# Performance work log

Hardware: AMD Instinct MI355X
Metric: run time of the kernel (lower is better)

The kernel has to match this reference:

```python
import jax, jax.numpy as jnp
import numpy as np

DIM = 2048
NUM_EXPERTS = 64
NUM_TOKENS = 16384
BETA = 0.5
EPSILON = 0.05
SINKHORN_ITER = 5
EPS_NORM = 1e-12  # torch F.normalize clamp


def setup_inputs() -> dict:
    key = jax.random.key(0)
    kx, ke = jax.random.split(key)
    x = jax.random.normal(kx, (NUM_TOKENS, DIM), dtype=jnp.float32)
    # orthogonal init for experts [E, dim]
    g = jax.random.normal(ke, (NUM_EXPERTS, DIM), dtype=jnp.float32)
    q, r = jnp.linalg.qr(g.T)  # [dim, E]
    experts = (q * jnp.sign(jnp.diag(r))).T  # [E, dim], orthonormal rows
    return {"x": x, "experts": experts}


def _l2_normalize(v, axis=-1):
    n = jnp.linalg.norm(v, axis=axis, keepdims=True)
    return v / jnp.maximum(n, EPS_NORM)


def _log_sinkhorn(cost, epsilon, iterations):
    B, E = cost.shape
    log_K = -cost / epsilon  # [B, E]
    log_col_mass = jnp.log(jnp.float32(B) / jnp.float32(E))

    def body(carry, _):
        log_u, log_v = carry
        log_u = -jax.nn.logsumexp(log_K + log_v[None, :], axis=1)  # [B]
        log_v = log_col_mass - jax.nn.logsumexp(log_K + log_u[:, None], axis=0)  # [E]
        return (log_u, log_v), None

    init = (jnp.zeros((B,), cost.dtype), jnp.zeros((E,), cost.dtype))
    (log_u, log_v), _ = jax.lax.scan(body, init, None, length=iterations)
    return log_K + log_u[:, None] + log_v[None, :]


def reference(x, experts):
    x_norm = _l2_normalize(x)          # [B, dim]
    e_norm = _l2_normalize(experts)    # [E, dim]
    sim = x_norm @ e_norm.T            # [B, E]
    gram = e_norm @ e_norm.T           # [E, E]
    gram_off = jax.nn.relu(gram - jnp.eye(NUM_EXPERTS, dtype=gram.dtype))
    repulsion = sim @ gram_off         # [B, E]
    score = sim - BETA * repulsion
    cost = -score
    log_P = _log_sinkhorn(cost, EPSILON, SINKHORN_ITER)
    probs = jnp.exp(log_P)
    return (probs, sim, gram, gram_off)
```

## Files before the change

kernel.cpp:

```cpp
#include <hip/hip_runtime.h>
#include <math.h>

#define TOKENS 16384
#define EXPERTS 64
#define DIM 2048
#define BETA 0.5f
#define EPSILON 0.05f
#define EPSN 1e-12f
#define LOGMASS 5.545177444479562f

#define OFF_ENORM   0
#define OFF_BBF     131072
#define OFF_M       262144
#define OFF_LOGK    266240
#define OFF_U       1314816
#define OFF_V       1331200
#define OFF_PART    1331264


typedef __attribute__((ext_vector_type(8))) short short8v;
typedef __attribute__((ext_vector_type(4))) float f32x4;

static __device__ __forceinline__ unsigned short f2bf(float f) {
  unsigned int u = __float_as_uint(f);
  u += 0x7FFFu + ((u >> 16) & 1u);
  return (unsigned short)(u >> 16);
}

__global__ __launch_bounds__(256) void k1_norm_experts(const float* __restrict__ ex,
                                                       float* __restrict__ ws) {
  int j = blockIdx.x, t = threadIdx.x;
  const float4* row4 = (const float4*)(ex + (size_t)j * DIM);
  float4 v0 = row4[t];
  float4 v1 = row4[t + 256];
  float ss = v0.x*v0.x + v0.y*v0.y + v0.z*v0.z + v0.w*v0.w
           + v1.x*v1.x + v1.y*v1.y + v1.z*v1.z + v1.w*v1.w;
  #pragma unroll
  for (int m = 1; m < 64; m <<= 1) ss += __shfl_xor(ss, m);
  __shared__ float red[4];
  int wv = t >> 6, ln = t & 63;
  if (ln == 0) red[wv] = ss;
  __syncthreads();
  float tot = red[0] + red[1] + red[2] + red[3];
  float sc = 1.0f / fmaxf(sqrtf(tot), EPSN);
  float4 w0 = make_float4(v0.x*sc, v0.y*sc, v0.z*sc, v0.w*sc);
  float4 w1 = make_float4(v1.x*sc, v1.y*sc, v1.z*sc, v1.w*sc);
  float4* en4 = (float4*)(ws + OFF_ENORM + (size_t)j * DIM);
  en4[t] = w0;
  en4[t + 256] = w1;
  unsigned short* Bb = (unsigned short*)(ws + OFF_BBF);
  int k0 = t * 4;
  int i0 = ((k0 >> 5) << 11) + (j << 5) + (k0 & 31);
  ushort4 u0; u0.x = f2bf(w0.x); u0.y = f2bf(w0.y); u0.z = f2bf(w0.z); u0.w = f2bf(w0.w);
  *(ushort4*)(Bb + i0) = u0;
  int k1v = (t + 256) * 4;
  int i1 = ((k1v >> 5) << 11) + (j << 5) + (k1v & 31);
  ushort4 u1; u1.x = f2bf(w1.x); u1.y = f2bf(w1.y); u1.z = f2bf(w1.z); u1.w = f2bf(w1.w);
  *(ushort4*)(Bb + i1) = u1;
}

__global__ __launch_bounds__(256) void k2_gram(const float* __restrict__ wsr,
                                               float* __restrict__ ws,
                                               float* __restrict__ out) {
  __shared__ __align__(16) float ej[DIM];
  __shared__ float part[4][64];
  int j = blockIdx.x, t = threadIdx.x;
  const float4* en4 = (const float4*)(wsr + OFF_ENORM + (size_t)j * DIM);
  ((float4*)ej)[t] = en4[t];
  ((float4*)ej)[t + 256] = en4[t + 256];
  __syncthreads();
  int kk = t & 63, q = t >> 6;
  const float4* er = (const float4*)(wsr + OFF_ENORM + (size_t)kk * DIM) + q * 128;
  const float4* ejq = (const float4*)ej + q * 128;
  float p = 0.f;
  #pragma unroll 4
  for (int i = 0; i < 128; ++i) {
    float4 a = ejq[i], b = er[i];
    p += a.x*b.x + a.y*b.y + a.z*b.z + a.w*b.w;
  }
  part[q][kk] = p;
  __syncthreads();
  if (t < 64) {
    float g = part[0][t] + part[1][t] + part[2][t] + part[3][t];
    out[2097152 + j*64 + t] = g;
    float go = fmaxf(g - (t == j ? 1.0f : 0.0f), 0.0f);
    out[2101248 + j*64 + t] = go;
    ws[OFF_M + j*64 + t] = (t == j ? 1.0f : 0.0f) - BETA * go;
  }
}

__global__ __launch_bounds__(256) void k3_main(const float* __restrict__ x,
                                               const float* __restrict__ wsr,
                                               float* __restrict__ ws,
                                               float* __restrict__ out) {
  __shared__ __align__(16) unsigned short A_lds[32 * 64];
  __shared__ __align__(16) float Ml[64 * 64];
  __shared__ __align__(16) float simL[32 * 68];
  __shared__ float sqL[32][8];
  __shared__ float scaleL[32];

  const int t = threadIdx.x;
  const int r0 = blockIdx.x * 32;

  const int srow = t >> 3;
  const int sk8  = (t & 7) << 3;
  const float* xrow = x + (size_t)(r0 + srow) * DIM + sk8;
  char* Ab = (char*)A_lds;
  const int wbyte = (srow * 128 + ((t & 7) << 4)) ^ ((srow & 7) << 4);

  const int l = t & 63, w = t >> 6;
  const int rw = w & 1;
  const int tcA = (w >> 1) << 1;
  const int arow = rw * 16 + (l & 15);
  const int abyte0 = (arow * 128 + ((l >> 4) << 4)) ^ ((arow & 7) << 4);
  const int abyte1 = (arow * 128 + ((4 + (l >> 4)) << 4)) ^ ((arow & 7) << 4);
  const unsigned short* Bws = (const unsigned short*)(wsr + OFF_BBF);
  const int boffA = ((tcA * 16 + (l & 15)) << 5) + ((l >> 4) << 3);
  const int boffB = boffA + (16 << 5);

  f32x4 acc0 = {0.f, 0.f, 0.f, 0.f};
  f32x4 acc1 = {0.f, 0.f, 0.f, 0.f};
  float nsq = 0.f;

  float4 a0 = *(const float4*)xrow;
  float4 a1 = *(const float4*)(xrow + 4);

  for (int c = 0; c < 32; ++c) {
    float4 c0 = a0, c1 = a1;
    if (c < 31) {
      const float* nx = xrow + (c + 1) * 64;
      a0 = *(const float4*)nx;
      a1 = *(const float4*)(nx + 4);
    }
    const unsigned short* bp = Bws + (size_t)(c * 2) * 2048;
    short8v b00 = *(const short8v*)(bp + boffA);
    short8v b01 = *(const short8v*)(bp + boffB);
    short8v b10 = *(const short8v*)(bp + 2048 + boffA);
    short8v b11 = *(const short8v*)(bp + 2048 + boffB);

    nsq += c0.x*c0.x + c0.y*c0.y + c0.z*c0.z + c0.w*c0.w
         + c1.x*c1.x + c1.y*c1.y + c1.z*c1.z + c1.w*c1.w;
    short8v av;
    av[0] = (short)f2bf(c0.x); av[1] = (short)f2bf(c0.y);
    av[2] = (short)f2bf(c0.z); av[3] = (short)f2bf(c0.w);
    av[4] = (short)f2bf(c1.x); av[5] = (short)f2bf(c1.y);
    av[6] = (short)f2bf(c1.z); av[7] = (short)f2bf(c1.w);
    *(short8v*)(Ab + wbyte) = av;
    __syncthreads();
    short8v af0 = *(const short8v*)(Ab + abyte0);
    short8v af1 = *(const short8v*)(Ab + abyte1);
    acc0 = __builtin_amdgcn_mfma_f32_16x16x32_bf16(af0, b00, acc0, 0, 0, 0);
    acc1 = __builtin_amdgcn_mfma_f32_16x16x32_bf16(af0, b01, acc1, 0, 0, 0);
    acc0 = __builtin_amdgcn_mfma_f32_16x16x32_bf16(af1, b10, acc0, 0, 0, 0);
    acc1 = __builtin_amdgcn_mfma_f32_16x16x32_bf16(af1, b11, acc1, 0, 0, 0);
    __syncthreads();
  }

  sqL[srow][t & 7] = nsq;
  {
    const float4* Mw = (const float4*)(wsr + OFF_M);
    float4* Ml4 = (float4*)Ml;
    #pragma unroll
    for (int s = 0; s < 4; ++s) Ml4[s * 256 + t] = Mw[s * 256 + t];
  }
  __syncthreads();
  if (t < 32) {
    float tot = 0.f;
    #pragma unroll
    for (int i = 0; i < 8; ++i) tot += sqL[t][i];
    scaleL[t] = 1.0f / fmaxf(sqrtf(tot), EPSN);
  }
  __syncthreads();

  float* simOut = out + 1048576;
  const int colA = tcA * 16 + (l & 15);
  #pragma unroll
  for (int j = 0; j < 4; ++j) {
    int rr = rw * 16 + ((l >> 4) << 2) + j;
    float sc = scaleL[rr];
    float s0 = acc0[j] * sc, s1 = acc1[j] * sc;
    simL[rr * 68 + colA]      = s0;
    simL[rr * 68 + colA + 16] = s1;
    simOut[(size_t)(r0 + rr) * 64 + colA]      = s0;
    simOut[(size_t)(r0 + rr) * 64 + colA + 16] = s1;
  }
  __syncthreads();

  const int tr = t >> 4, tc = t & 15;
  float lk0[4] = {0.f,0.f,0.f,0.f}, lk1[4] = {0.f,0.f,0.f,0.f};
  #pragma unroll 8
  for (int j = 0; j < 64; ++j) {
    float4 mj = *(const float4*)&Ml[j * 64 + (tc << 2)];
    float s0 = simL[(tr * 2) * 68 + j];
    float s1 = simL[(tr * 2 + 1) * 68 + j];
    lk0[0] += s0*mj.x; lk0[1] += s0*mj.y; lk0[2] += s0*mj.z; lk0[3] += s0*mj.w;
    lk1[0] += s1*mj.x; lk1[1] += s1*mj.y; lk1[2] += s1*mj.z; lk1[3] += s1*mj.w;
  }
  float* logK = ws + OFF_LOGK;
  const float ie = 1.0f / EPSILON;
  float4 o0 = make_float4(lk0[0]*ie, lk0[1]*ie, lk0[2]*ie, lk0[3]*ie);
  float4 o1 = make_float4(lk1[0]*ie, lk1[1]*ie, lk1[2]*ie, lk1[3]*ie);
  *(float4*)(logK + (size_t)(r0 + tr*2    ) * 64 + (tc << 2)) = o0;
  *(float4*)(logK + (size_t)(r0 + tr*2 + 1) * 64 + (tc << 2)) = o1;
}

__global__ __launch_bounds__(256) void k4_iter(const float* __restrict__ wsr,
                                               float* __restrict__ ws, int use_v) {
  const float* logK = wsr + OFF_LOGK;
  const float* vg = wsr + OFF_V;
  float* u = ws + OFF_U;
  float* part = ws + OFF_PART;
  __shared__ float vL[64];
  __shared__ float cpm[4][64], cps[4][64];
  int t = threadIdx.x, b = blockIdx.x;
  if (t < 64) vL[t] = use_v ? vg[t] : 0.0f;
  __syncthreads();
  int rloc = t >> 2, q = t & 3;
  int row = b * 64 + rloc;
  const float4* lr = (const float4*)(logK + (size_t)row * 64 + q * 16);
  float4 A0 = lr[0], A1 = lr[1], A2 = lr[2], A3 = lr[3];
  float r[16] = {A0.x,A0.y,A0.z,A0.w, A1.x,A1.y,A1.z,A1.w,
                 A2.x,A2.y,A2.z,A2.w, A3.x,A3.y,A3.z,A3.w};
  float m = -3.402823466e38f;
  #pragma unroll
  for (int i = 0; i < 16; ++i) m = fmaxf(m, r[i] + vL[q * 16 + i]);
  m = fmaxf(m, __shfl_xor(m, 1));
  m = fmaxf(m, __shfl_xor(m, 2));
  float s = 0.f;
  #pragma unroll
  for (int i = 0; i < 16; ++i) s += __expf(r[i] + vL[q * 16 + i] - m);
  s += __shfl_xor(s, 1);
  s += __shfl_xor(s, 2);
  float urow = -(m + __logf(s));
  if (q == 0) u[row] = urow;
  float cm[16], cs[16];
  #pragma unroll
  for (int i = 0; i < 16; ++i) cm[i] = r[i] + urow;
  #pragma unroll
  for (int i = 0; i < 16; ++i) {
    float mm = cm[i];
    mm = fmaxf(mm, __shfl_xor(mm, 4));
    mm = fmaxf(mm, __shfl_xor(mm, 8));
    mm = fmaxf(mm, __shfl_xor(mm, 16));
    mm = fmaxf(mm, __shfl_xor(mm, 32));
    float e = __expf(cm[i] - mm);
    e += __shfl_xor(e, 4);
    e += __shfl_xor(e, 8);
    e += __shfl_xor(e, 16);
    e += __shfl_xor(e, 32);
    cm[i] = mm; cs[i] = e;
  }
  int wv = t >> 6, ll = t & 63;
  if (ll < 4) {
    #pragma unroll
    for (int i = 0; i < 16; ++i) { cpm[wv][ll*16+i] = cm[i]; cps[wv][ll*16+i] = cs[i]; }
  }
  __syncthreads();
  if (t < 64) {
    float M2 = cpm[0][t], S2 = cps[0][t];
    #pragma unroll
    for (int w2 = 1; w2 < 4; ++w2) {
      float pm = cpm[w2][t], ps = cps[w2][t];
      float nm = fmaxf(M2, pm);
      S2 = S2 * __expf(M2 - nm) + ps * __expf(pm - nm);
      M2 = nm;
    }
    part[(size_t)(b * 64 + t) * 2]     = M2;
    part[(size_t)(b * 64 + t) * 2 + 1] = S2;
  }
}

__global__ __launch_bounds__(256) void k5_combine(const float* __restrict__ wsr,
                                                  float* __restrict__ ws) {
  const float* part = wsr + OFF_PART;
  float* v = ws + OFF_V;
  __shared__ float pm_[4][64], ps_[4][64];
  int t = threadIdx.x;
  int j = t & 63, g = t >> 6;
  float m = -3.402823466e38f, s = 0.0f;
  for (int b0 = g * 64; b0 < g * 64 + 64; b0 += 8) {
    float pm[8], ps[8];
    #pragma unroll
    for (int i = 0; i < 8; ++i) {
      pm[i] = part[(size_t)((b0 + i) * 64 + j) * 2];
      ps[i] = part[(size_t)((b0 + i) * 64 + j) * 2 + 1];
    }
    #pragma unroll
    for (int i = 0; i < 8; ++i) {
      float nm = fmaxf(m, pm[i]);
      s = s * __expf(m - nm) + ps[i] * __expf(pm[i] - nm);
      m = nm;
    }
  }
  pm_[g][j] = m; ps_[g][j] = s;
  __syncthreads();
  if (t < 64) {
    float M2 = pm_[0][t], S2 = ps_[0][t];
    #pragma unroll
    for (int w = 1; w < 4; ++w) {
      float pm = pm_[w][t], ps = ps_[w][t];
      float nm = fmaxf(M2, pm);
      S2 = S2 * __expf(M2 - nm) + ps * __expf(pm - nm);
      M2 = nm;
    }
    v[t] = LOGMASS - (M2 + __logf(S2));
  }
}

__global__ __launch_bounds__(256) void k7_final(const float* __restrict__ wsr,
                                                float* __restrict__ out) {
  const float* logK = wsr + OFF_LOGK;
  const float* u = wsr + OFF_U;
  const float* v = wsr + OFF_V;
  int idx = blockIdx.x * 256 + threadIdx.x;
  int e = idx << 2;
  int row = e >> 6, col = e & 63;
  float4 lk = *(const float4*)(logK + e);
  float ur = u[row];
  float4 vv = *(const float4*)(v + col);
  float4 o = make_float4(__expf(lk.x + ur + vv.x), __expf(lk.y + ur + vv.y),
                         __expf(lk.z + ur + vv.z), __expf(lk.w + ur + vv.w));
  *(float4*)(out + e) = o;
}

extern "C" void kernel_launch(void* const* d_in, const int* in_sizes, int n_in,
                              void* d_out, int out_size, void* d_ws, size_t ws_size,
                              hipStream_t stream) {
  const float* x  = (const float*)d_in[0];
  const float* ex = (const float*)d_in[1];
  float* out = (float*)d_out;
  float* ws  = (float*)d_ws;

  k1_norm_experts<<<64, 256, 0, stream>>>(ex, ws);
  k2_gram<<<64, 256, 0, stream>>>(ws, ws, out);
  k3_main<<<512, 256, 0, stream>>>(x, ws, ws, out);
  for (int it = 0; it < 5; ++it) {
    k4_iter<<<256, 256, 0, stream>>>(ws, ws, it > 0 ? 1 : 0);
    k5_combine<<<1, 256, 0, stream>>>(ws, ws);
  }
  k7_final<<<1024, 256, 0, stream>>>(ws, out);
}
```

Baseline: 271.7 us.

## Fuse Sinkhorn iterations into one cooperative kernel using linear-domain scaling

Replaces the ten per-iteration launches (row pass plus column combine) and the final exp kernel with a single cooperative kernel. Each thread keeps its logK slice in registers as exp(logK), and iterations run with plain multiplies and reciprocals instead of log-sum-exp. Column sums are gathered with atomics and a grid-wide sync. This removes launch overhead and repeated logK reads, but linear-domain scaling can overflow or underflow when logK values are large (cost/0.05 can reach about 20+), and atomic summation order is nondeterministic.

Measured after the change: 373.1 us. 1.37x slower.

```diff
diff --git a/kernel.cpp b/kernel.cpp
--- a/kernel.cpp
+++ b/kernel.cpp
@@ -1,5 +1,8 @@
 #include <hip/hip_runtime.h>
+#include <hip/hip_cooperative_groups.h>
 #include <math.h>
+
+namespace cg = cooperative_groups;
 
 #define TOKENS 16384
 #define EXPERTS 64
@@ -7,15 +10,13 @@
 #define BETA 0.5f
 #define EPSILON 0.05f
 #define EPSN 1e-12f
-#define LOGMASS 5.545177444479562f
+#define COLMASS 256.0f
 
 #define OFF_ENORM   0
 #define OFF_BBF     131072
 #define OFF_M       262144
 #define OFF_LOGK    266240
-#define OFF_U       1314816
-#define OFF_V       1331200
-#define OFF_PART    1331264
+#define OFF_COLS    1314816
 
 
 typedef __attribute__((ext_vector_type(8))) short short8v;
@@ -30,6 +31,7 @@
 __global__ __launch_bounds__(256) void k1_norm_experts(const float* __restrict__ ex,
                                                        float* __restrict__ ws) {
   int j = blockIdx.x, t = threadIdx.x;
+  if (j < 5 && t < 64) ws[OFF_COLS + j * 64 + t] = 0.0f;
   const float4* row4 = (const float4*)(ex + (size_t)j * DIM);
   float4 v0 = row4[t];
   float4 v1 = row4[t + 256];
@@ -204,123 +206,71 @@
   *(float4*)(logK + (size_t)(r0 + tr*2 + 1) * 64 + (tc << 2)) = o1;
 }
 
-__global__ __launch_bounds__(256) void k4_iter(const float* __restrict__ wsr,
-                                               float* __restrict__ ws, int use_v) {
-  const float* logK = wsr + OFF_LOGK;
-  const float* vg = wsr + OFF_V;
-  float* u = ws + OFF_U;
-  float* part = ws + OFF_PART;
-  __shared__ float vL[64];
-  __shared__ float cpm[4][64], cps[4][64];
-  int t = threadIdx.x, b = blockIdx.x;
-  if (t < 64) vL[t] = use_v ? vg[t] : 0.0f;
-  __syncthreads();
-  int rloc = t >> 2, q = t & 3;
-  int row = b * 64 + rloc;
+__global__ __launch_bounds__(256) void kS_sinkhorn(const float* __restrict__ logK,
+                                                   float* __restrict__ colsums,
+                                                   float* __restrict__ out) {
+  cg::grid_group grid = cg::this_grid();
+  __shared__ float cps[4][64];
+  __shared__ float cL[64];
+  const int t = threadIdx.x, b = blockIdx.x;
+  const int q = t & 3;
+  const int row = b * 64 + (t >> 2);
   const float4* lr = (const float4*)(logK + (size_t)row * 64 + q * 16);
   float4 A0 = lr[0], A1 = lr[1], A2 = lr[2], A3 = lr[3];
-  float r[16] = {A0.x,A0.y,A0.z,A0.w, A1.x,A1.y,A1.z,A1.w,
+  float k[16] = {A0.x,A0.y,A0.z,A0.w, A1.x,A1.y,A1.z,A1.w,
                  A2.x,A2.y,A2.z,A2.w, A3.x,A3.y,A3.z,A3.w};
-  float m = -3.402823466e38f;
-  #pragma unroll
-  for (int i = 0; i < 16; ++i) m = fmaxf(m, r[i] + vL[q * 16 + i]);
-  m = fmaxf(m, __shfl_xor(m, 1));
-  m = fmaxf(m, __shfl_xor(m, 2));
-  float s = 0.f;
-  #pragma unroll
-  for (int i = 0; i < 16; ++i) s += __expf(r[i] + vL[q * 16 + i] - m);
-  s += __shfl_xor(s, 1);
-  s += __shfl_xor(s, 2);
-  float urow = -(m + __logf(s));
-  if (q == 0) u[row] = urow;
-  float cm[16], cs[16];
-  #pragma unroll
-  for (int i = 0; i < 16; ++i) cm[i] = r[i] + urow;
-  #pragma unroll
-  for (int i = 0; i < 16; ++i) {
-    float mm = cm[i];
-    mm = fmaxf(mm, __shfl_xor(mm, 4));
-    mm = fmaxf(mm, __shfl_xor(mm, 8));
-    mm = fmaxf(mm, __shfl_xor(mm, 16));
-    mm = fmaxf(mm, __shfl_xor(mm, 32));
-    float e = __expf(cm[i] - mm);
-    e += __shfl_xor(e, 4);
-    e += __shfl_xor(e, 8);
-    e += __shfl_xor(e, 16);
-    e += __shfl_xor(e, 32);
-    cm[i] = mm; cs[i] = e;
-  }
-  int wv = t >> 6, ll = t & 63;
-  if (ll < 4) {
-    #pragma unroll
-    for (int i = 0; i < 16; ++i) { cpm[wv][ll*16+i] = cm[i]; cps[wv][ll*16+i] = cs[i]; }
-  }
-  __syncthreads();
-  if (t < 64) {
-    float M2 = cpm[0][t], S2 = cps[0][t];
-    #pragma unroll
-    for (int w2 = 1; w2 < 4; ++w2) {
-      float pm = cpm[w2][t], ps = cps[w2][t];
-      float nm = fmaxf(M2, pm);
-      S2 = S2 * __expf(M2 - nm) + ps * __expf(pm - nm);
-      M2 = nm;
-    }
-    part[(size_t)(b * 64 + t) * 2]     = M2;
-    part[(size_t)(b * 64 + t) * 2 + 1] = S2;
-  }
-}
-
-__global__ __launch_bounds__(256) void k5_combine(const float* __restrict__ wsr,
-                                                  float* __restrict__ ws) {
-  const float* part = wsr + OFF_PART;
-  float* v = ws + OFF_V;
-  __shared__ float pm_[4][64], ps_[4][64];
-  int t = threadIdx.x;
-  int j = t & 63, g = t >> 6;
-  float m = -3.402823466e38f, s = 0.0f;
-  for (int b0 = g * 64; b0 < g * 64 + 64; b0 += 8) {
-    float pm[8], ps[8];
-    #pragma unroll
-    for (int i = 0; i < 8; ++i) {
-      pm[i] = part[(size_t)((b0 + i) * 64 + j) * 2];
-      ps[i] = part[(size_t)((b0 + i) * 64 + j) * 2 + 1];
-    }
-    #pragma unroll
-    for (int i = 0; i < 8; ++i) {
-      float nm = fmaxf(m, pm[i]);
-      s = s * __expf(m - nm) + ps[i] * __expf(pm[i] - nm);
-      m = nm;
-    }
-  }
-  pm_[g][j] = m; ps_[g][j] = s;
-  __syncthreads();
-  if (t < 64) {
-    float M2 = pm_[0][t], S2 = ps_[0][t];
-    #pragma unroll
-    for (int w = 1; w < 4; ++w) {
-      float pm = pm_[w][t], ps = ps_[w][t];
-      float nm = fmaxf(M2, pm);
-      S2 = S2 * __expf(M2 - nm) + ps * __expf(pm - nm);
-      M2 = nm;
-    }
-    v[t] = LOGMASS - (M2 + __logf(S2));
-  }
-}
-
-__global__ __launch_bounds__(256) void k7_final(const float* __restrict__ wsr,
-                                                float* __restrict__ out) {
-  const float* logK = wsr + OFF_LOGK;
-  const float* u = wsr + OFF_U;
-  const float* v = wsr + OFF_V;
-  int idx = blockIdx.x * 256 + threadIdx.x;
-  int e = idx << 2;
-  int row = e >> 6, col = e & 63;
-  float4 lk = *(const float4*)(logK + e);
-  float ur = u[row];
-  float4 vv = *(const float4*)(v + col);
-  float4 o = make_float4(__expf(lk.x + ur + vv.x), __expf(lk.y + ur + vv.y),
-                         __expf(lk.z + ur + vv.z), __expf(lk.w + ur + vv.w));
-  *(float4*)(out + e) = o;
+  #pragma unroll
+  for (int i = 0; i < 16; ++i) k[i] = __expf(k[i]);
+  float c[16];
+  #pragma unroll
+  for (int i = 0; i < 16; ++i) c[i] = 1.0f;
+  float u = 0.f;
+
+  for (int it = 0; it < 5; ++it) {
+    float s = 0.f;
+    #pragma unroll
+    for (int i = 0; i < 16; ++i) s += k[i] * c[i];
+    s += __shfl_xor(s, 1);
+    s += __shfl_xor(s, 2);
+    u = 1.0f / s;
+    float pc[16];
+    #pragma unroll
+    for (int i = 0; i < 16; ++i) pc[i] = k[i] * u;
+    #pragma unroll
+    for (int i = 0; i < 16; ++i) {
+      pc[i] += __shfl_xor(pc[i], 4);
+      pc[i] += __shfl_xor(pc[i], 8);
+      pc[i] += __shfl_xor(pc[i], 16);
+      pc[i] += __shfl_xor(pc[i], 32);
+    }
+    const int wv = t >> 6, l = t & 63;
+    if (l < 4) {
+      #pragma unroll
+      for (int i = 0; i < 16; ++i) cps[wv][l * 16 + i] = pc[i];
+    }
+    __syncthreads();
+    if (t < 64) {
+      float tot = cps[0][t] + cps[1][t] + cps[2][t] + cps[3][t];
+      atomicAdd(&colsums[it * 64 + t], tot);
+    }
+    grid.sync();
+    if (t < 64) {
+      volatile const float* cv = colsums + it * 64;
+      cL[t] = COLMASS / cv[t];
+    }
+    __syncthreads();
+    #pragma unroll
+    for (int i = 0; i < 16; ++i) c[i] = cL[q * 16 + i];
+  }
+
+  float p[16];
+  #pragma unroll
+  for (int i = 0; i < 16; ++i) p[i] = u * k[i] * c[i];
+  float4* op = (float4*)(out + (size_t)row * 64 + q * 16);
+  op[0] = make_float4(p[0], p[1], p[2], p[3]);
+  op[1] = make_float4(p[4], p[5], p[6], p[7]);
+  op[2] = make_float4(p[8], p[9], p[10], p[11]);
+  op[3] = make_float4(p[12], p[13], p[14], p[15]);
 }
 
 extern "C" void kernel_launch(void* const* d_in, const int* in_sizes, int n_in,
@@ -334,9 +284,10 @@
   k1_norm_experts<<<64, 256, 0, stream>>>(ex, ws);
   k2_gram<<<64, 256, 0, stream>>>(ws, ws, out);
   k3_main<<<512, 256, 0, stream>>>(x, ws, ws, out);
-  for (int it = 0; it < 5; ++it) {
-    k4_iter<<<256, 256, 0, stream>>>(ws, ws, it > 0 ? 1 : 0);
-    k5_combine<<<1, 256, 0, stream>>>(ws, ws);
-  }
-  k7_final<<<1024, 256, 0, stream>>>(ws, out);
-}
+
+  const float* logK = ws + OFF_LOGK;
+  float* cols = ws + OFF_COLS;
+  void* args[] = { (void*)&logK, (void*)&cols, (void*)&out };
+  hipLaunchCooperativeKernel((const void*)kS_sinkhorn, dim3(256), dim3(256),
+                             args, 0, stream);
+}
```
